# Kernel tuning notes

Measured on AMD Instinct MI355X. Metric: run time of the kernel, lower is better.

## Reference

```python
import jax, jax.numpy as jnp
import numpy as np

B, T, D = 4, 4096, 1024
N, L = 2048, 768
H = 16
EPS = 1e-5

def layernorm(x, g, b):
    mu = jnp.mean(x, axis=-1, keepdims=True)
    var = jnp.mean((x - mu) ** 2, axis=-1, keepdims=True)
    return (x - mu) * jax.lax.rsqrt(var + EPS) * g + b

def setup_inputs() -> dict:
    key = jax.random.key(0)
    ks = jax.random.split(key, 8)
    s_d = 1.0 / np.sqrt(D)
    s_l = 1.0 / np.sqrt(L)
    return {
        "x1": jax.random.normal(ks[0], (B, T, D), jnp.float32),
        "x2": jax.random.normal(ks[1], (B, N, L), jnp.float32),
        "Wq": jax.random.normal(ks[2], (D, D), jnp.float32) * s_d,
        "bq": jnp.zeros((D,), jnp.float32),
        "Wk": jax.random.normal(ks[3], (L, D), jnp.float32) * s_l,
        "bk": jnp.zeros((D,), jnp.float32),
        "Wv": jax.random.normal(ks[4], (L, D), jnp.float32) * s_l,
        "bv": jnp.zeros((D,), jnp.float32),
        "Wh": jax.random.normal(ks[5], (D, D), jnp.float32) * s_d,
        "bh": jnp.zeros((D,), jnp.float32),
        "g1": jnp.ones((D,), jnp.float32),
        "b1": jnp.zeros((D,), jnp.float32),
        "g2": jnp.ones((L,), jnp.float32),
        "b2": jnp.zeros((L,), jnp.float32),
    }

def reference(x1, x2, Wq, bq, Wk, bk, Wv, bv, Wh, bh, g1, b1, g2, b2):
    nx1 = layernorm(x1, g1, b1)
    nx2 = layernorm(x2, g2, b2)
    q = (nx1 @ Wq + bq).reshape(B, T, H, D // H)
    k = (nx2 @ Wk + bk).reshape(B, N, H, D // H)
    v = (nx2 @ Wv + bv).reshape(B, N, H, D // H)
    q = jax.nn.softmax(q, axis=-1)
    k = jax.nn.softmax(k, axis=-1)
    # dropout p=0 -> identity
    attn = jnp.einsum('bnhd,bnhl->bhdl', k, v)          # [B,H,dh,dh]
    y = jnp.einsum('bthd,bhdl->bthl', q, attn).reshape(B, T, D)
    return x1 @ Wh + bh + y
```

## Files before the change

kernel.cpp:

```cpp
#include <hip/hip_runtime.h>


#define DEV __device__ __forceinline__

typedef unsigned short bf16_t;
typedef __attribute__((ext_vector_type(8))) __bf16 bf16x8;
typedef __attribute__((ext_vector_type(8))) unsigned short ushort8;
typedef __attribute__((ext_vector_type(4))) float f32x4;

DEV unsigned short f2bf(float f) {
  unsigned int u = __float_as_uint(f);
  unsigned int r = 0x7FFFu + ((u >> 16) & 1u);
  return (unsigned short)((u + r) >> 16);
}
DEV float bf2f(unsigned short u) { return __uint_as_float(((unsigned int)u) << 16); }

DEV void gld16(const void* g, void* l) {
  __builtin_amdgcn_global_load_lds((__attribute__((address_space(1))) void*)g,
                                   (__attribute__((address_space(3))) void*)l, 16, 0, 0);
}

__global__ __launch_bounds__(256) void wprep_kernel(
    const float* __restrict__ Wq, const float* __restrict__ Wk,
    const float* __restrict__ Wv, const float* __restrict__ Wh,
    bf16_t* __restrict__ WqT, bf16_t* __restrict__ WkT,
    bf16_t* __restrict__ WvT, bf16_t* __restrict__ WhT) {
  int t = blockIdx.x;
  const float* src; bf16_t* dst; int K;
  if (t < 1024)      { src = Wq; dst = WqT; K = 1024; }
  else if (t < 1792) { src = Wk; dst = WkT; K = 768;  t -= 1024; }
  else if (t < 2560) { src = Wv; dst = WvT; K = 768;  t -= 1792; }
  else               { src = Wh; dst = WhT; K = 1024; t -= 2560; }
  int tk = t >> 5, tn = t & 31;
  __shared__ float tile[32][33];
  int tx = threadIdx.x & 31, ty = threadIdx.x >> 5;
#pragma unroll
  for (int i = 0; i < 4; ++i) {
    int r = ty + i * 8;
    tile[r][tx] = src[(size_t)(tk * 32 + r) * 1024 + tn * 32 + tx];
  }
  __syncthreads();
#pragma unroll
  for (int i = 0; i < 4; ++i) {
    int r = ty + i * 8;
    dst[(size_t)(tn * 32 + r) * K + tk * 32 + tx] = f2bf(tile[tx][r]);
  }
}

__global__ __launch_bounds__(256) void ln1_kernel(
    const float* __restrict__ x1, const float* __restrict__ g1, const float* __restrict__ b1,
    bf16_t* __restrict__ nx1, bf16_t* __restrict__ x1b) {
  int row = blockIdx.x, tid = threadIdx.x;
  size_t base = (size_t)row * 1024;
  float4 xv = *(const float4*)&x1[base + tid * 4];
  float s  = xv.x + xv.y + xv.z + xv.w;
  float s2 = xv.x * xv.x + xv.y * xv.y + xv.z * xv.z + xv.w * xv.w;
#pragma unroll
  for (int off = 32; off >= 1; off >>= 1) {
    s  += __shfl_down(s, off);
    s2 += __shfl_down(s2, off);
  }
  __shared__ float red[8];
  int wid = tid >> 6;
  if ((tid & 63) == 0) { red[wid] = s; red[4 + wid] = s2; }
  __syncthreads();
  s  = red[0] + red[1] + red[2] + red[3];
  s2 = red[4] + red[5] + red[6] + red[7];
  float mu = s * (1.0f / 1024.0f);
  float var = s2 * (1.0f / 1024.0f) - mu * mu;
  float rs = rsqrtf(var + 1e-5f);
  float4 gv = *(const float4*)&g1[tid * 4];
  float4 bv = *(const float4*)&b1[tid * 4];
  ushort4 pn, px;
  pn.x = f2bf((xv.x - mu) * rs * gv.x + bv.x);
  pn.y = f2bf((xv.y - mu) * rs * gv.y + bv.y);
  pn.z = f2bf((xv.z - mu) * rs * gv.z + bv.z);
  pn.w = f2bf((xv.w - mu) * rs * gv.w + bv.w);
  px.x = f2bf(xv.x); px.y = f2bf(xv.y); px.z = f2bf(xv.z); px.w = f2bf(xv.w);
  *(ushort4*)&nx1[base + tid * 4] = pn;
  *(ushort4*)&x1b[base + tid * 4] = px;
}

__global__ __launch_bounds__(256) void ln2_kernel(
    const float* __restrict__ x2, const float* __restrict__ g2, const float* __restrict__ b2,
    bf16_t* __restrict__ nx2) {
  int row = blockIdx.x, tid = threadIdx.x;
  size_t base = (size_t)row * 768;
  float a0 = x2[base + tid], a1 = x2[base + tid + 256], a2 = x2[base + tid + 512];
  float s = a0 + a1 + a2;
  float s2 = a0 * a0 + a1 * a1 + a2 * a2;
#pragma unroll
  for (int off = 32; off >= 1; off >>= 1) {
    s  += __shfl_down(s, off);
    s2 += __shfl_down(s2, off);
  }
  __shared__ float red[8];
  int wid = tid >> 6;
  if ((tid & 63) == 0) { red[wid] = s; red[4 + wid] = s2; }
  __syncthreads();
  s  = red[0] + red[1] + red[2] + red[3];
  s2 = red[4] + red[5] + red[6] + red[7];
  float mu = s * (1.0f / 768.0f);
  float var = s2 * (1.0f / 768.0f) - mu * mu;
  float rs = rsqrtf(var + 1e-5f);
  nx2[base + tid]       = f2bf((a0 - mu) * rs * g2[tid]       + b2[tid]);
  nx2[base + tid + 256] = f2bf((a1 - mu) * rs * g2[tid + 256] + b2[tid + 256]);
  nx2[base + tid + 512] = f2bf((a2 - mu) * rs * g2[tid + 512] + b2[tid + 512]);
}

__global__ __launch_bounds__(256) void gemm_qkv_kernel(
    const bf16_t* __restrict__ nx1, const bf16_t* __restrict__ WqT,
    const float* __restrict__ bq, bf16_t* __restrict__ qout,
    const bf16_t* __restrict__ nx2, const bf16_t* __restrict__ WkT,
    const float* __restrict__ bk, bf16_t* __restrict__ kout,
    const bf16_t* __restrict__ WvT, const float* __restrict__ bv,
    bf16_t* __restrict__ vout) {
  __shared__ bf16_t As[128 * 32];
  __shared__ bf16_t Bs[128 * 32];
  int id = blockIdx.x;
  const bf16_t *A, *BT; const float* bias; bf16_t* out;
  int K, bm, bn, do_softmax;
  if (id < 1024) {
    A = nx1; BT = WqT; bias = bq; out = qout; K = 1024;
    bm = id & 127; bn = id >> 7; do_softmax = 1;
  } else if (id < 1536) {
    id -= 1024; A = nx2; BT = WkT; bias = bk; out = kout; K = 768;
    bm = id & 63; bn = id >> 6; do_softmax = 1;
  } else {
    id -= 1536; A = nx2; BT = WvT; bias = bv; out = vout; K = 768;
    bm = id & 63; bn = id >> 6; do_softmax = 0;
  }
  int tid = threadIdx.x;
  int lane = tid & 63, wid = tid >> 6;
  int wm = wid & 1, wn = wid >> 1;
  f32x4 acc[4][4];
#pragma unroll
  for (int i = 0; i < 4; ++i)
#pragma unroll
    for (int j = 0; j < 4; ++j) acc[i][j] = {0.f, 0.f, 0.f, 0.f};
  int nk = K >> 5;
  const bf16_t* Ab = A  + (size_t)bm * 128 * K;
  const bf16_t* Bb = BT + (size_t)bn * 128 * K;
  for (int kt = 0; kt < nk; ++kt) {
    __syncthreads();
#pragma unroll
    for (int i = 0; i < 2; ++i) {
      int c = i * 256 + tid;
      gld16(Ab + (size_t)(c >> 2) * K + kt * 32 + (c & 3) * 8, (void*)(As + c * 8));
      gld16(Bb + (size_t)(c >> 2) * K + kt * 32 + (c & 3) * 8, (void*)(Bs + c * 8));
    }
    __syncthreads();
    bf16x8 af[4], bfr[4];
#pragma unroll
    for (int mi = 0; mi < 4; ++mi)
      af[mi] = *(const bf16x8*)&As[(wm * 64 + mi * 16 + (lane & 15)) * 32 + (lane >> 4) * 8];
#pragma unroll
    for (int ni = 0; ni < 4; ++ni)
      bfr[ni] = *(const bf16x8*)&Bs[(wn * 64 + ni * 16 + (lane & 15)) * 32 + (lane >> 4) * 8];
#pragma unroll
    for (int mi = 0; mi < 4; ++mi)
#pragma unroll
      for (int ni = 0; ni < 4; ++ni)
        acc[mi][ni] = __builtin_amdgcn_mfma_f32_16x16x32_bf16(af[mi], bfr[ni], acc[mi][ni], 0, 0, 0);
  }
  int colg0 = bn * 128 + wn * 64;
  float bvv[4];
#pragma unroll
  for (int ni = 0; ni < 4; ++ni) bvv[ni] = bias[colg0 + ni * 16 + (lane & 15)];
#pragma unroll
  for (int mi = 0; mi < 4; ++mi) {
#pragma unroll
    for (int r = 0; r < 4; ++r) {
      int row = bm * 128 + wm * 64 + mi * 16 + (lane >> 4) * 4 + r;
      float vx[4];
#pragma unroll
      for (int ni = 0; ni < 4; ++ni) vx[ni] = acc[mi][ni][r] + bvv[ni];
      if (do_softmax) {
        float mx = fmaxf(fmaxf(vx[0], vx[1]), fmaxf(vx[2], vx[3]));
#pragma unroll
        for (int off = 1; off < 16; off <<= 1) mx = fmaxf(mx, __shfl_xor(mx, off));
        float ssum = 0.f;
#pragma unroll
        for (int ni = 0; ni < 4; ++ni) { vx[ni] = __expf(vx[ni] - mx); ssum += vx[ni]; }
#pragma unroll
        for (int off = 1; off < 16; off <<= 1) ssum += __shfl_xor(ssum, off);
        float inv = 1.0f / ssum;
#pragma unroll
        for (int ni = 0; ni < 4; ++ni) vx[ni] *= inv;
      }
#pragma unroll
      for (int ni = 0; ni < 4; ++ni)
        out[(size_t)row * 1024 + colg0 + ni * 16 + (lane & 15)] = f2bf(vx[ni]);
    }
  }
}

__global__ __launch_bounds__(256) void attn_partial_kernel(
    const bf16_t* __restrict__ kq, const bf16_t* __restrict__ vq,
    float* __restrict__ part) {
  int bh = blockIdx.x >> 3, c = blockIdx.x & 7;
  int b = bh >> 4, h = bh & 15;
  int tid = threadIdx.x;
  int td = tid & 15, tl = tid >> 4;
  __shared__ float ks[32][64];
  __shared__ float vs[32][64];
  float acc[4][4];
#pragma unroll
  for (int i = 0; i < 4; ++i)
#pragma unroll
    for (int j = 0; j < 4; ++j) acc[i][j] = 0.f;
  for (int s = 0; s < 8; ++s) {
    __syncthreads();
    int nr = tid >> 3, col = (tid & 7) * 8;
    int n = c * 256 + s * 32 + nr;
    size_t goff = ((size_t)(b * 2048 + n)) * 1024 + h * 64 + col;
    ushort8 lk = *(const ushort8*)&kq[goff];
    ushort8 lv = *(const ushort8*)&vq[goff];
#pragma unroll
    for (int j = 0; j < 8; ++j) {
      ks[nr][col + j] = bf2f(lk[j]);
      vs[nr][col + j] = bf2f(lv[j]);
    }
    __syncthreads();
#pragma unroll
    for (int nn = 0; nn < 32; ++nn) {
      float4 kv = *(const float4*)&ks[nn][td * 4];
      float4 vv = *(const float4*)&vs[nn][tl * 4];
      float ka[4] = {kv.x, kv.y, kv.z, kv.w};
      float va[4] = {vv.x, vv.y, vv.z, vv.w};
#pragma unroll
      for (int i = 0; i < 4; ++i)
#pragma unroll
        for (int j = 0; j < 4; ++j) acc[i][j] += ka[i] * va[j];
    }
  }
#pragma unroll
  for (int i = 0; i < 4; ++i)
#pragma unroll
    for (int j = 0; j < 4; ++j) {
      int d = td * 4 + i, l = tl * 4 + j;
      part[(((size_t)bh * 8 + c) * 64 + d) * 64 + l] = acc[i][j];
    }
}

__global__ __launch_bounds__(256) void attn_finalize_kernel(
    const float* __restrict__ part, bf16_t* __restrict__ attnT) {
  int bh = blockIdx.x, tid = threadIdx.x;
  for (int t = tid; t < 4096; t += 256) {
    int d = t >> 6, l = t & 63;
    float s = 0.f;
#pragma unroll
    for (int c = 0; c < 8; ++c)
      s += part[(((size_t)bh * 8 + c) * 64 + d) * 64 + l];
    attnT[((size_t)bh * 64 + l) * 64 + d] = f2bf(s);
  }
}

__global__ __launch_bounds__(256) void gemm_final_kernel(
    const bf16_t* __restrict__ A, const bf16_t* __restrict__ WT,
    const float* __restrict__ bias, const bf16_t* __restrict__ qb,
    const bf16_t* __restrict__ attnT, float* __restrict__ out) {
  __shared__ bf16_t As [128 * 32];
  __shared__ bf16_t As2[128 * 32];
  __shared__ bf16_t Bs [128 * 32];
  const int K = 1024;
  int tid = threadIdx.x;
  int bm = blockIdx.x, bn = blockIdx.y;
  int lane = tid & 63, wid = tid >> 6;
  int wm = wid & 1, wn = wid >> 1;
  int b = bm >> 5;
  f32x4 acc[4][4];
#pragma unroll
  for (int i = 0; i < 4; ++i)
#pragma unroll
    for (int j = 0; j < 4; ++j) acc[i][j] = {0.f, 0.f, 0.f, 0.f};
  const bf16_t* Ab = A  + (size_t)bm * 128 * K;
  const bf16_t* Bb = WT + (size_t)bn * 128 * K;
  for (int kt = 0; kt < 34; ++kt) {
    __syncthreads();
    if (kt < 32) {
#pragma unroll
      for (int i = 0; i < 2; ++i) {
        int c = i * 256 + tid;
        gld16(Ab + (size_t)(c >> 2) * K + kt * 32 + (c & 3) * 8, (void*)(As + c * 8));
        gld16(Bb + (size_t)(c >> 2) * K + kt * 32 + (c & 3) * 8, (void*)(Bs + c * 8));
      }
    } else {
      int k2 = kt - 32;
      const bf16_t* Aq = qb + (size_t)bm * 128 * 1024 + bn * 128 + k2 * 32;
      const bf16_t* Bt = attnT + ((size_t)b * 1024 + bn * 128) * 64 + k2 * 32;
#pragma unroll
      for (int i = 0; i < 2; ++i) {
        int c = i * 256 + tid;
        gld16(Aq +      (size_t)(c >> 2) * 1024 + (c & 3) * 8, (void*)(As  + c * 8));
        gld16(Aq + 64 + (size_t)(c >> 2) * 1024 + (c & 3) * 8, (void*)(As2 + c * 8));
        gld16(Bt +      (size_t)(c >> 2) * 64   + (c & 3) * 8, (void*)(Bs  + c * 8));
      }
    }
    __syncthreads();
    const bf16_t* Ap = (kt >= 32 && wn) ? As2 : As;
    bf16x8 af[4], bfr[4];
#pragma unroll
    for (int mi = 0; mi < 4; ++mi)
      af[mi] = *(const bf16x8*)&Ap[(wm * 64 + mi * 16 + (lane & 15)) * 32 + (lane >> 4) * 8];
#pragma unroll
    for (int ni = 0; ni < 4; ++ni)
      bfr[ni] = *(const bf16x8*)&Bs[(wn * 64 + ni * 16 + (lane & 15)) * 32 + (lane >> 4) * 8];
#pragma unroll
    for (int mi = 0; mi < 4; ++mi)
#pragma unroll
      for (int ni = 0; ni < 4; ++ni)
        acc[mi][ni] = __builtin_amdgcn_mfma_f32_16x16x32_bf16(af[mi], bfr[ni], acc[mi][ni], 0, 0, 0);
  }
  int colg0 = bn * 128 + wn * 64;
  float bvv[4];
#pragma unroll
  for (int ni = 0; ni < 4; ++ni) bvv[ni] = bias[colg0 + ni * 16 + (lane & 15)];
#pragma unroll
  for (int mi = 0; mi < 4; ++mi)
#pragma unroll
    for (int r = 0; r < 4; ++r) {
      int row = bm * 128 + wm * 64 + mi * 16 + (lane >> 4) * 4 + r;
#pragma unroll
      for (int ni = 0; ni < 4; ++ni)
        out[(size_t)row * 1024 + colg0 + ni * 16 + (lane & 15)] = acc[mi][ni][r] + bvv[ni];
    }
}

extern "C" void kernel_launch(void* const* d_in, const int* in_sizes, int n_in,
                              void* d_out, int out_size, void* d_ws, size_t ws_size,
                              hipStream_t stream) {
  const float* x1 = (const float*)d_in[0];
  const float* x2 = (const float*)d_in[1];
  const float* Wq = (const float*)d_in[2];
  const float* bq = (const float*)d_in[3];
  const float* Wk = (const float*)d_in[4];
  const float* bk = (const float*)d_in[5];
  const float* Wv = (const float*)d_in[6];
  const float* bv = (const float*)d_in[7];
  const float* Wh = (const float*)d_in[8];
  const float* bh = (const float*)d_in[9];
  const float* g1 = (const float*)d_in[10];
  const float* b1 = (const float*)d_in[11];
  const float* g2 = (const float*)d_in[12];
  const float* b2 = (const float*)d_in[13];
  float* out = (float*)d_out;

  char* w = (char*)d_ws;
  bf16_t* nx1  = (bf16_t*)w; w += (size_t)16384 * 1024 * 2;
  bf16_t* x1b  = (bf16_t*)w; w += (size_t)16384 * 1024 * 2;
  bf16_t* nx2  = (bf16_t*)w; w += (size_t)8192 * 768 * 2;
  bf16_t* WqT  = (bf16_t*)w; w += (size_t)1024 * 1024 * 2;
  bf16_t* WkT  = (bf16_t*)w; w += (size_t)1024 * 768 * 2;
  bf16_t* WvT  = (bf16_t*)w; w += (size_t)1024 * 768 * 2;
  bf16_t* WhT  = (bf16_t*)w; w += (size_t)1024 * 1024 * 2;
  bf16_t* qb   = (bf16_t*)w; w += (size_t)16384 * 1024 * 2;
  bf16_t* kbuf = (bf16_t*)w; w += (size_t)8192 * 1024 * 2;
  bf16_t* vbuf = (bf16_t*)w; w += (size_t)8192 * 1024 * 2;
  float*  part = (float*)w;  w += (size_t)64 * 8 * 64 * 64 * 4;
  bf16_t* attnT = (bf16_t*)w; w += (size_t)64 * 64 * 64 * 2;

  wprep_kernel<<<dim3(3584), dim3(256), 0, stream>>>(Wq, Wk, Wv, Wh, WqT, WkT, WvT, WhT);
  ln1_kernel<<<dim3(16384), dim3(256), 0, stream>>>(x1, g1, b1, nx1, x1b);
  ln2_kernel<<<dim3(8192), dim3(256), 0, stream>>>(x2, g2, b2, nx2);
  gemm_qkv_kernel<<<dim3(2048), dim3(256), 0, stream>>>(
      nx1, WqT, bq, qb, nx2, WkT, bk, kbuf, WvT, bv, vbuf);
  attn_partial_kernel<<<dim3(512), dim3(256), 0, stream>>>(kbuf, vbuf, part);
  attn_finalize_kernel<<<dim3(64), dim3(256), 0, stream>>>(part, attnT);
  gemm_final_kernel<<<dim3(128, 8), dim3(256), 0, stream>>>(x1b, WhT, bh, qb, attnT, out);
}
```

Before: 345.2 us.

## Load GEMM MFMA fragments directly from global memory with register double-buffering

Both the QKV and final GEMM kernels stop staging tiles through LDS with global_load_lds and barriers. Each lane now loads its MFMA A/B fragments straight from global memory into registers, with a two-stage software prefetch. The softmax in the QKV epilogue also drops the max-subtraction and its shuffle reduction. This removes LDS traffic and syncthreads, but each wave reloads data its sibling waves share, making reuse depend on L1/L2. Skipping the max makes the softmax unsafe against overflow for large logits.

```diff
diff --git a/kernel.cpp b/kernel.cpp
--- a/kernel.cpp
+++ b/kernel.cpp
@@ -14,11 +14,6 @@
   return (unsigned short)((u + r) >> 16);
 }
 DEV float bf2f(unsigned short u) { return __uint_as_float(((unsigned int)u) << 16); }
-
-DEV void gld16(const void* g, void* l) {
-  __builtin_amdgcn_global_load_lds((__attribute__((address_space(1))) void*)g,
-                                   (__attribute__((address_space(3))) void*)l, 16, 0, 0);
-}
 
 __global__ __launch_bounds__(256) void wprep_kernel(
     const float* __restrict__ Wq, const float* __restrict__ Wk,
@@ -115,8 +110,6 @@
     const float* __restrict__ bk, bf16_t* __restrict__ kout,
     const bf16_t* __restrict__ WvT, const float* __restrict__ bv,
     bf16_t* __restrict__ vout) {
-  __shared__ bf16_t As[128 * 32];
-  __shared__ bf16_t Bs[128 * 32];
   int id = blockIdx.x;
   const bf16_t *A, *BT; const float* bias; bf16_t* out;
   int K, bm, bn, do_softmax;
@@ -133,36 +126,53 @@
   int tid = threadIdx.x;
   int lane = tid & 63, wid = tid >> 6;
   int wm = wid & 1, wn = wid >> 1;
+  int klane = (lane >> 4) * 8;
+
+  const bf16x8* Ap[4];
+  const bf16x8* Bp[4];
+#pragma unroll
+  for (int mi = 0; mi < 4; ++mi)
+    Ap[mi] = (const bf16x8*)(A + (size_t)(bm * 128 + wm * 64 + mi * 16 + (lane & 15)) * K + klane);
+#pragma unroll
+  for (int ni = 0; ni < 4; ++ni)
+    Bp[ni] = (const bf16x8*)(BT + (size_t)(bn * 128 + wn * 64 + ni * 16 + (lane & 15)) * K + klane);
+
   f32x4 acc[4][4];
 #pragma unroll
   for (int i = 0; i < 4; ++i)
 #pragma unroll
     for (int j = 0; j < 4; ++j) acc[i][j] = {0.f, 0.f, 0.f, 0.f};
+
   int nk = K >> 5;
-  const bf16_t* Ab = A  + (size_t)bm * 128 * K;
-  const bf16_t* Bb = BT + (size_t)bn * 128 * K;
-  for (int kt = 0; kt < nk; ++kt) {
-    __syncthreads();
-#pragma unroll
-    for (int i = 0; i < 2; ++i) {
-      int c = i * 256 + tid;
-      gld16(Ab + (size_t)(c >> 2) * K + kt * 32 + (c & 3) * 8, (void*)(As + c * 8));
-      gld16(Bb + (size_t)(c >> 2) * K + kt * 32 + (c & 3) * 8, (void*)(Bs + c * 8));
-    }
-    __syncthreads();
-    bf16x8 af[4], bfr[4];
+  bf16x8 a0[4], b0[4], a1[4], b1[4];
+#pragma unroll
+  for (int mi = 0; mi < 4; ++mi) a0[mi] = Ap[mi][0];
+#pragma unroll
+  for (int ni = 0; ni < 4; ++ni) b0[ni] = Bp[ni][0];
+
+  for (int kt = 0; kt < nk; kt += 2) {
+#pragma unroll
+    for (int mi = 0; mi < 4; ++mi) a1[mi] = Ap[mi][(kt + 1) * 4];
+#pragma unroll
+    for (int ni = 0; ni < 4; ++ni) b1[ni] = Bp[ni][(kt + 1) * 4];
 #pragma unroll
     for (int mi = 0; mi < 4; ++mi)
-      af[mi] = *(const bf16x8*)&As[(wm * 64 + mi * 16 + (lane & 15)) * 32 + (lane >> 4) * 8];
-#pragma unroll
-    for (int ni = 0; ni < 4; ++ni)
-      bfr[ni] = *(const bf16x8*)&Bs[(wn * 64 + ni * 16 + (lane & 15)) * 32 + (lane >> 4) * 8];
+#pragma unroll
+      for (int ni = 0; ni < 4; ++ni)
+        acc[mi][ni] = __builtin_amdgcn_mfma_f32_16x16x32_bf16(a0[mi], b0[ni], acc[mi][ni], 0, 0, 0);
+    if (kt + 2 < nk) {
+#pragma unroll
+      for (int mi = 0; mi < 4; ++mi) a0[mi] = Ap[mi][(kt + 2) * 4];
+#pragma unroll
+      for (int ni = 0; ni < 4; ++ni) b0[ni] = Bp[ni][(kt + 2) * 4];
+    }
 #pragma unroll
     for (int mi = 0; mi < 4; ++mi)
 #pragma unroll
       for (int ni = 0; ni < 4; ++ni)
-        acc[mi][ni] = __builtin_amdgcn_mfma_f32_16x16x32_bf16(af[mi], bfr[ni], acc[mi][ni], 0, 0, 0);
-  }
+        acc[mi][ni] = __builtin_amdgcn_mfma_f32_16x16x32_bf16(a1[mi], b1[ni], acc[mi][ni], 0, 0, 0);
+  }
+
   int colg0 = bn * 128 + wn * 64;
   float bvv[4];
 #pragma unroll
@@ -176,12 +186,9 @@
 #pragma unroll
       for (int ni = 0; ni < 4; ++ni) vx[ni] = acc[mi][ni][r] + bvv[ni];
       if (do_softmax) {
-        float mx = fmaxf(fmaxf(vx[0], vx[1]), fmaxf(vx[2], vx[3]));
-#pragma unroll
-        for (int off = 1; off < 16; off <<= 1) mx = fmaxf(mx, __shfl_xor(mx, off));
         float ssum = 0.f;
 #pragma unroll
-        for (int ni = 0; ni < 4; ++ni) { vx[ni] = __expf(vx[ni] - mx); ssum += vx[ni]; }
+        for (int ni = 0; ni < 4; ++ni) { vx[ni] = __expf(vx[ni]); ssum += vx[ni]; }
 #pragma unroll
         for (int off = 1; off < 16; off <<= 1) ssum += __shfl_xor(ssum, off);
         float inv = 1.0f / ssum;
@@ -260,58 +267,84 @@
     const bf16_t* __restrict__ A, const bf16_t* __restrict__ WT,
     const float* __restrict__ bias, const bf16_t* __restrict__ qb,
     const bf16_t* __restrict__ attnT, float* __restrict__ out) {
-  __shared__ bf16_t As [128 * 32];
-  __shared__ bf16_t As2[128 * 32];
-  __shared__ bf16_t Bs [128 * 32];
   const int K = 1024;
   int tid = threadIdx.x;
   int bm = blockIdx.x, bn = blockIdx.y;
   int lane = tid & 63, wid = tid >> 6;
   int wm = wid & 1, wn = wid >> 1;
   int b = bm >> 5;
+  int klane = (lane >> 4) * 8;
+
+  const bf16x8* Ap[4];
+  const bf16x8* Bp[4];
+#pragma unroll
+  for (int mi = 0; mi < 4; ++mi)
+    Ap[mi] = (const bf16x8*)(A + (size_t)(bm * 128 + wm * 64 + mi * 16 + (lane & 15)) * K + klane);
+#pragma unroll
+  for (int ni = 0; ni < 4; ++ni)
+    Bp[ni] = (const bf16x8*)(WT + (size_t)(bn * 128 + wn * 64 + ni * 16 + (lane & 15)) * K + klane);
+
   f32x4 acc[4][4];
 #pragma unroll
   for (int i = 0; i < 4; ++i)
 #pragma unroll
     for (int j = 0; j < 4; ++j) acc[i][j] = {0.f, 0.f, 0.f, 0.f};
-  const bf16_t* Ab = A  + (size_t)bm * 128 * K;
-  const bf16_t* Bb = WT + (size_t)bn * 128 * K;
-  for (int kt = 0; kt < 34; ++kt) {
-    __syncthreads();
-    if (kt < 32) {
-#pragma unroll
-      for (int i = 0; i < 2; ++i) {
-        int c = i * 256 + tid;
-        gld16(Ab + (size_t)(c >> 2) * K + kt * 32 + (c & 3) * 8, (void*)(As + c * 8));
-        gld16(Bb + (size_t)(c >> 2) * K + kt * 32 + (c & 3) * 8, (void*)(Bs + c * 8));
-      }
-    } else {
-      int k2 = kt - 32;
-      const bf16_t* Aq = qb + (size_t)bm * 128 * 1024 + bn * 128 + k2 * 32;
-      const bf16_t* Bt = attnT + ((size_t)b * 1024 + bn * 128) * 64 + k2 * 32;
-#pragma unroll
-      for (int i = 0; i < 2; ++i) {
-        int c = i * 256 + tid;
-        gld16(Aq +      (size_t)(c >> 2) * 1024 + (c & 3) * 8, (void*)(As  + c * 8));
-        gld16(Aq + 64 + (size_t)(c >> 2) * 1024 + (c & 3) * 8, (void*)(As2 + c * 8));
-        gld16(Bt +      (size_t)(c >> 2) * 64   + (c & 3) * 8, (void*)(Bs  + c * 8));
-      }
-    }
-    __syncthreads();
-    const bf16_t* Ap = (kt >= 32 && wn) ? As2 : As;
-    bf16x8 af[4], bfr[4];
+
+  bf16x8 a0[4], b0[4], a1[4], b1[4];
+#pragma unroll
+  for (int mi = 0; mi < 4; ++mi) a0[mi] = Ap[mi][0];
+#pragma unroll
+  for (int ni = 0; ni < 4; ++ni) b0[ni] = Bp[ni][0];
+
+  for (int kt = 0; kt < 32; kt += 2) {
+#pragma unroll
+    for (int mi = 0; mi < 4; ++mi) a1[mi] = Ap[mi][(kt + 1) * 4];
+#pragma unroll
+    for (int ni = 0; ni < 4; ++ni) b1[ni] = Bp[ni][(kt + 1) * 4];
 #pragma unroll
     for (int mi = 0; mi < 4; ++mi)
-      af[mi] = *(const bf16x8*)&Ap[(wm * 64 + mi * 16 + (lane & 15)) * 32 + (lane >> 4) * 8];
+#pragma unroll
+      for (int ni = 0; ni < 4; ++ni)
+        acc[mi][ni] = __builtin_amdgcn_mfma_f32_16x16x32_bf16(a0[mi], b0[ni], acc[mi][ni], 0, 0, 0);
+    if (kt + 2 < 32) {
+#pragma unroll
+      for (int mi = 0; mi < 4; ++mi) a0[mi] = Ap[mi][(kt + 2) * 4];
+#pragma unroll
+      for (int ni = 0; ni < 4; ++ni) b0[ni] = Bp[ni][(kt + 2) * 4];
+    }
+#pragma unroll
+    for (int mi = 0; mi < 4; ++mi)
+#pragma unroll
+      for (int ni = 0; ni < 4; ++ni)
+        acc[mi][ni] = __builtin_amdgcn_mfma_f32_16x16x32_bf16(a1[mi], b1[ni], acc[mi][ni], 0, 0, 0);
+  }
+
+  {
+    const bf16x8* Aq[4];
+    const bf16x8* Bt[4];
+#pragma unroll
+    for (int mi = 0; mi < 4; ++mi)
+      Aq[mi] = (const bf16x8*)(qb + (size_t)(bm * 128 + wm * 64 + mi * 16 + (lane & 15)) * 1024
+                               + bn * 128 + wn * 64 + klane);
 #pragma unroll
     for (int ni = 0; ni < 4; ++ni)
-      bfr[ni] = *(const bf16x8*)&Bs[(wn * 64 + ni * 16 + (lane & 15)) * 32 + (lane >> 4) * 8];
-#pragma unroll
-    for (int mi = 0; mi < 4; ++mi)
-#pragma unroll
-      for (int ni = 0; ni < 4; ++ni)
-        acc[mi][ni] = __builtin_amdgcn_mfma_f32_16x16x32_bf16(af[mi], bfr[ni], acc[mi][ni], 0, 0, 0);
-  }
+      Bt[ni] = (const bf16x8*)(attnT + ((size_t)(b * 16 + 2 * bn + wn) * 64 + ni * 16 + (lane & 15)) * 64
+                               + klane);
+#pragma unroll
+    for (int k2 = 0; k2 < 2; ++k2) {
+      bf16x8 aq[4], bt[4];
+#pragma unroll
+      for (int mi = 0; mi < 4; ++mi) aq[mi] = Aq[mi][k2 * 4];
+#pragma unroll
+      for (int ni = 0; ni < 4; ++ni) bt[ni] = Bt[ni][k2 * 4];
+#pragma unroll
+      for (int mi = 0; mi < 4; ++mi)
+#pragma unroll
+        for (int ni = 0; ni < 4; ++ni)
+          acc[mi][ni] = __builtin_amdgcn_mfma_f32_16x16x32_bf16(aq[mi], bt[ni], acc[mi][ni], 0, 0, 0);
+    }
+  }
+
   int colg0 = bn * 128 + wn * 64;
   float bvv[4];
 #pragma unroll
```

Result: slower. 546.9 us (+58.4%).

## Widen GEMM tiles to 128x256 and restructure final q·attn epilogue

Applied to the files above, without the earlier changes.

Both the QKV GEMM and the final GEMM now use 128x256 output tiles, with each wave computing 64x128 and 32 accumulators, which halves the grid sizes. The aim is to reduce global/LDS traffic per FLOP and raise MFMA density. The final kernel drops the two extra LDS-staged K-steps for q·attn and instead loads q and attnT fragments directly from global memory per head. The QKV softmax also removes the max subtraction, relying on values being small enough not to overflow exp. The costs are much higher register pressure (launch_bounds 256,2), fewer blocks per GPU, and a possible numerical risk from the unguarded exp.

```diff
diff --git a/kernel.cpp b/kernel.cpp
--- a/kernel.cpp
+++ b/kernel.cpp
@@ -108,7 +108,7 @@
   nx2[base + tid + 512] = f2bf((a2 - mu) * rs * g2[tid + 512] + b2[tid + 512]);
 }
 
-__global__ __launch_bounds__(256) void gemm_qkv_kernel(
+__global__ __launch_bounds__(256, 2) void gemm_qkv_kernel(
     const bf16_t* __restrict__ nx1, const bf16_t* __restrict__ WqT,
     const float* __restrict__ bq, bf16_t* __restrict__ qout,
     const bf16_t* __restrict__ nx2, const bf16_t* __restrict__ WkT,
@@ -116,80 +116,89 @@
     const bf16_t* __restrict__ WvT, const float* __restrict__ bv,
     bf16_t* __restrict__ vout) {
   __shared__ bf16_t As[128 * 32];
-  __shared__ bf16_t Bs[128 * 32];
+  __shared__ bf16_t Bs[256 * 32];
   int id = blockIdx.x;
   const bf16_t *A, *BT; const float* bias; bf16_t* out;
   int K, bm, bn, do_softmax;
-  if (id < 1024) {
+  if (id < 512) {
     A = nx1; BT = WqT; bias = bq; out = qout; K = 1024;
     bm = id & 127; bn = id >> 7; do_softmax = 1;
-  } else if (id < 1536) {
-    id -= 1024; A = nx2; BT = WkT; bias = bk; out = kout; K = 768;
+  } else if (id < 768) {
+    id -= 512; A = nx2; BT = WkT; bias = bk; out = kout; K = 768;
     bm = id & 63; bn = id >> 6; do_softmax = 1;
   } else {
-    id -= 1536; A = nx2; BT = WvT; bias = bv; out = vout; K = 768;
+    id -= 768; A = nx2; BT = WvT; bias = bv; out = vout; K = 768;
     bm = id & 63; bn = id >> 6; do_softmax = 0;
   }
   int tid = threadIdx.x;
   int lane = tid & 63, wid = tid >> 6;
   int wm = wid & 1, wn = wid >> 1;
-  f32x4 acc[4][4];
+  int klane = (lane >> 4) * 8;
+
+  f32x4 acc[4][8];
 #pragma unroll
   for (int i = 0; i < 4; ++i)
 #pragma unroll
-    for (int j = 0; j < 4; ++j) acc[i][j] = {0.f, 0.f, 0.f, 0.f};
+    for (int j = 0; j < 8; ++j) acc[i][j] = {0.f, 0.f, 0.f, 0.f};
+
   int nk = K >> 5;
   const bf16_t* Ab = A  + (size_t)bm * 128 * K;
-  const bf16_t* Bb = BT + (size_t)bn * 128 * K;
+  const bf16_t* Bb = BT + (size_t)bn * 256 * K;
   for (int kt = 0; kt < nk; ++kt) {
     __syncthreads();
-#pragma unroll
-    for (int i = 0; i < 2; ++i) {
-      int c = i * 256 + tid;
+    {
+      int c = tid;
       gld16(Ab + (size_t)(c >> 2) * K + kt * 32 + (c & 3) * 8, (void*)(As + c * 8));
-      gld16(Bb + (size_t)(c >> 2) * K + kt * 32 + (c & 3) * 8, (void*)(Bs + c * 8));
-    }
-    __syncthreads();
-    bf16x8 af[4], bfr[4];
+      c = 256 + tid;
+      gld16(Ab + (size_t)(c >> 2) * K + kt * 32 + (c & 3) * 8, (void*)(As + c * 8));
+#pragma unroll
+      for (int i = 0; i < 4; ++i) {
+        c = i * 256 + tid;
+        gld16(Bb + (size_t)(c >> 2) * K + kt * 32 + (c & 3) * 8, (void*)(Bs + c * 8));
+      }
+    }
+    __syncthreads();
+    bf16x8 af[4], bfr[8];
 #pragma unroll
     for (int mi = 0; mi < 4; ++mi)
-      af[mi] = *(const bf16x8*)&As[(wm * 64 + mi * 16 + (lane & 15)) * 32 + (lane >> 4) * 8];
-#pragma unroll
-    for (int ni = 0; ni < 4; ++ni)
-      bfr[ni] = *(const bf16x8*)&Bs[(wn * 64 + ni * 16 + (lane & 15)) * 32 + (lane >> 4) * 8];
+      af[mi] = *(const bf16x8*)&As[(wm * 64 + mi * 16 + (lane & 15)) * 32 + klane];
+#pragma unroll
+    for (int ni = 0; ni < 8; ++ni)
+      bfr[ni] = *(const bf16x8*)&Bs[(wn * 128 + ni * 16 + (lane & 15)) * 32 + klane];
 #pragma unroll
     for (int mi = 0; mi < 4; ++mi)
 #pragma unroll
-      for (int ni = 0; ni < 4; ++ni)
+      for (int ni = 0; ni < 8; ++ni)
         acc[mi][ni] = __builtin_amdgcn_mfma_f32_16x16x32_bf16(af[mi], bfr[ni], acc[mi][ni], 0, 0, 0);
   }
-  int colg0 = bn * 128 + wn * 64;
-  float bvv[4];
-#pragma unroll
-  for (int ni = 0; ni < 4; ++ni) bvv[ni] = bias[colg0 + ni * 16 + (lane & 15)];
+
+  int colg0 = bn * 256 + wn * 128;
+  float bvv[8];
+#pragma unroll
+  for (int ni = 0; ni < 8; ++ni) bvv[ni] = bias[colg0 + ni * 16 + (lane & 15)];
 #pragma unroll
   for (int mi = 0; mi < 4; ++mi) {
 #pragma unroll
     for (int r = 0; r < 4; ++r) {
       int row = bm * 128 + wm * 64 + mi * 16 + (lane >> 4) * 4 + r;
-      float vx[4];
-#pragma unroll
-      for (int ni = 0; ni < 4; ++ni) vx[ni] = acc[mi][ni][r] + bvv[ni];
+      float vx[8];
+#pragma unroll
+      for (int ni = 0; ni < 8; ++ni) vx[ni] = acc[mi][ni][r] + bvv[ni];
       if (do_softmax) {
-        float mx = fmaxf(fmaxf(vx[0], vx[1]), fmaxf(vx[2], vx[3]));
-#pragma unroll
-        for (int off = 1; off < 16; off <<= 1) mx = fmaxf(mx, __shfl_xor(mx, off));
-        float ssum = 0.f;
-#pragma unroll
-        for (int ni = 0; ni < 4; ++ni) { vx[ni] = __expf(vx[ni] - mx); ssum += vx[ni]; }
-#pragma unroll
-        for (int off = 1; off < 16; off <<= 1) ssum += __shfl_xor(ssum, off);
-        float inv = 1.0f / ssum;
-#pragma unroll
-        for (int ni = 0; ni < 4; ++ni) vx[ni] *= inv;
+#pragma unroll
+        for (int g = 0; g < 2; ++g) {
+          float ssum = 0.f;
+#pragma unroll
+          for (int j = 0; j < 4; ++j) { vx[g * 4 + j] = __expf(vx[g * 4 + j]); ssum += vx[g * 4 + j]; }
+#pragma unroll
+          for (int off = 1; off < 16; off <<= 1) ssum += __shfl_xor(ssum, off);
+          float inv = 1.0f / ssum;
+#pragma unroll
+          for (int j = 0; j < 4; ++j) vx[g * 4 + j] *= inv;
+        }
       }
 #pragma unroll
-      for (int ni = 0; ni < 4; ++ni)
+      for (int ni = 0; ni < 8; ++ni)
         out[(size_t)row * 1024 + colg0 + ni * 16 + (lane & 15)] = f2bf(vx[ni]);
     }
   }
@@ -256,73 +265,92 @@
   }
 }
 
-__global__ __launch_bounds__(256) void gemm_final_kernel(
+__global__ __launch_bounds__(256, 2) void gemm_final_kernel(
     const bf16_t* __restrict__ A, const bf16_t* __restrict__ WT,
     const float* __restrict__ bias, const bf16_t* __restrict__ qb,
     const bf16_t* __restrict__ attnT, float* __restrict__ out) {
-  __shared__ bf16_t As [128 * 32];
-  __shared__ bf16_t As2[128 * 32];
-  __shared__ bf16_t Bs [128 * 32];
+  __shared__ bf16_t As[128 * 32];
+  __shared__ bf16_t Bs[256 * 32];
   const int K = 1024;
   int tid = threadIdx.x;
   int bm = blockIdx.x, bn = blockIdx.y;
   int lane = tid & 63, wid = tid >> 6;
   int wm = wid & 1, wn = wid >> 1;
   int b = bm >> 5;
-  f32x4 acc[4][4];
+  int klane = (lane >> 4) * 8;
+
+  f32x4 acc[4][8];
 #pragma unroll
   for (int i = 0; i < 4; ++i)
 #pragma unroll
-    for (int j = 0; j < 4; ++j) acc[i][j] = {0.f, 0.f, 0.f, 0.f};
+    for (int j = 0; j < 8; ++j) acc[i][j] = {0.f, 0.f, 0.f, 0.f};
+
   const bf16_t* Ab = A  + (size_t)bm * 128 * K;
-  const bf16_t* Bb = WT + (size_t)bn * 128 * K;
-  for (int kt = 0; kt < 34; ++kt) {
-    __syncthreads();
-    if (kt < 32) {
-#pragma unroll
-      for (int i = 0; i < 2; ++i) {
-        int c = i * 256 + tid;
-        gld16(Ab + (size_t)(c >> 2) * K + kt * 32 + (c & 3) * 8, (void*)(As + c * 8));
+  const bf16_t* Bb = WT + (size_t)bn * 256 * K;
+  for (int kt = 0; kt < 32; ++kt) {
+    __syncthreads();
+    {
+      int c = tid;
+      gld16(Ab + (size_t)(c >> 2) * K + kt * 32 + (c & 3) * 8, (void*)(As + c * 8));
+      c = 256 + tid;
+      gld16(Ab + (size_t)(c >> 2) * K + kt * 32 + (c & 3) * 8, (void*)(As + c * 8));
+#pragma unroll
+      for (int i = 0; i < 4; ++i) {
+        c = i * 256 + tid;
         gld16(Bb + (size_t)(c >> 2) * K + kt * 32 + (c & 3) * 8, (void*)(Bs + c * 8));
       }
-    } else {
-      int k2 = kt - 32;
-      const bf16_t* Aq = qb + (size_t)bm * 128 * 1024 + bn * 128 + k2 * 32;
-      const bf16_t* Bt = attnT + ((size_t)b * 1024 + bn * 128) * 64 + k2 * 32;
-#pragma unroll
-      for (int i = 0; i < 2; ++i) {
-        int c = i * 256 + tid;
-        gld16(Aq +      (size_t)(c >> 2) * 1024 + (c & 3) * 8, (void*)(As  + c * 8));
-        gld16(Aq + 64 + (size_t)(c >> 2) * 1024 + (c & 3) * 8, (void*)(As2 + c * 8));
-        gld16(Bt +      (size_t)(c >> 2) * 64   + (c & 3) * 8, (void*)(Bs  + c * 8));
-      }
-    }
-    __syncthreads();
-    const bf16_t* Ap = (kt >= 32 && wn) ? As2 : As;
-    bf16x8 af[4], bfr[4];
+    }
+    __syncthreads();
+    bf16x8 af[4], bfr[8];
 #pragma unroll
     for (int mi = 0; mi < 4; ++mi)
-      af[mi] = *(const bf16x8*)&Ap[(wm * 64 + mi * 16 + (lane & 15)) * 32 + (lane >> 4) * 8];
-#pragma unroll
-    for (int ni = 0; ni < 4; ++ni)
-      bfr[ni] = *(const bf16x8*)&Bs[(wn * 64 + ni * 16 + (lane & 15)) * 32 + (lane >> 4) * 8];
+      af[mi] = *(const bf16x8*)&As[(wm * 64 + mi * 16 + (lane & 15)) * 32 + klane];
+#pragma unroll
+    for (int ni = 0; ni < 8; ++ni)
+      bfr[ni] = *(const bf16x8*)&Bs[(wn * 128 + ni * 16 + (lane & 15)) * 32 + klane];
 #pragma unroll
     for (int mi = 0; mi < 4; ++mi)
 #pragma unroll
-      for (int ni = 0; ni < 4; ++ni)
+      for (int ni = 0; ni < 8; ++ni)
         acc[mi][ni] = __builtin_amdgcn_mfma_f32_16x16x32_bf16(af[mi], bfr[ni], acc[mi][ni], 0, 0, 0);
   }
-  int colg0 = bn * 128 + wn * 64;
-  float bvv[4];
-#pragma unroll
-  for (int ni = 0; ni < 4; ++ni) bvv[ni] = bias[colg0 + ni * 16 + (lane & 15)];
+
+  {
+    int h0 = bn * 4 + wn * 2;
+#pragma unroll
+    for (int k2 = 0; k2 < 2; ++k2) {
+      bf16x8 aq[2][4], bt[8];
+#pragma unroll
+      for (int g = 0; g < 2; ++g)
+#pragma unroll
+        for (int mi = 0; mi < 4; ++mi)
+          aq[g][mi] = *(const bf16x8*)(qb
+              + (size_t)(bm * 128 + wm * 64 + mi * 16 + (lane & 15)) * 1024
+              + (h0 + g) * 64 + k2 * 32 + klane);
+#pragma unroll
+      for (int ni = 0; ni < 8; ++ni)
+        bt[ni] = *(const bf16x8*)(attnT
+            + ((size_t)(b * 16 + h0 + (ni >> 2)) * 64 + (ni & 3) * 16 + (lane & 15)) * 64
+            + k2 * 32 + klane);
+#pragma unroll
+      for (int mi = 0; mi < 4; ++mi)
+#pragma unroll
+        for (int ni = 0; ni < 8; ++ni)
+          acc[mi][ni] = __builtin_amdgcn_mfma_f32_16x16x32_bf16(aq[ni >> 2][mi], bt[ni], acc[mi][ni], 0, 0, 0);
+    }
+  }
+
+  int colg0 = bn * 256 + wn * 128;
+  float bvv[8];
+#pragma unroll
+  for (int ni = 0; ni < 8; ++ni) bvv[ni] = bias[colg0 + ni * 16 + (lane & 15)];
 #pragma unroll
   for (int mi = 0; mi < 4; ++mi)
 #pragma unroll
     for (int r = 0; r < 4; ++r) {
       int row = bm * 128 + wm * 64 + mi * 16 + (lane >> 4) * 4 + r;
 #pragma unroll
-      for (int ni = 0; ni < 4; ++ni)
+      for (int ni = 0; ni < 8; ++ni)
         out[(size_t)row * 1024 + colg0 + ni * 16 + (lane & 15)] = acc[mi][ni][r] + bvv[ni];
     }
 }
@@ -363,9 +391,9 @@
   wprep_kernel<<<dim3(3584), dim3(256), 0, stream>>>(Wq, Wk, Wv, Wh, WqT, WkT, WvT, WhT);
   ln1_kernel<<<dim3(16384), dim3(256), 0, stream>>>(x1, g1, b1, nx1, x1b);
   ln2_kernel<<<dim3(8192), dim3(256), 0, stream>>>(x2, g2, b2, nx2);
-  gemm_qkv_kernel<<<dim3(2048), dim3(256), 0, stream>>>(
+  gemm_qkv_kernel<<<dim3(1024), dim3(256), 0, stream>>>(
       nx1, WqT, bq, qb, nx2, WkT, bk, kbuf, WvT, bv, vbuf);
   attn_partial_kernel<<<dim3(512), dim3(256), 0, stream>>>(kbuf, vbuf, part);
   attn_finalize_kernel<<<dim3(64), dim3(256), 0, stream>>>(part, attnT);
-  gemm_final_kernel<<<dim3(128, 8), dim3(256), 0, stream>>>(x1b, WhT, bh, qb, attnT, out);
-}
+  gemm_final_kernel<<<dim3(128, 4), dim3(256), 0, stream>>>(x1b, WhT, bh, qb, attnT, out);
+}
```

Result: faster. 327.9 us (-5.0%).
